# Optimization experiments

Measured on AMD Instinct MI355X. Metric: run time of the kernel, lower is better.

The kernel has to match this reference:

```python
import jax, jax.numpy as jnp
import numpy as np

IN_FEATURES = 256
OUT_FEATURES = 128
ALPHA = 0.2  # LeakyReLU negative slope
NEG_INF = -9e15
N_NODES = 8192


def _xavier_uniform(key, shape, gain):
    fan_in, fan_out = shape[0], shape[1]
    limit = gain * np.sqrt(6.0 / (fan_in + fan_out))
    return jax.random.uniform(key, shape, jnp.float32, -limit, limit)


def setup_inputs() -> dict:
    key = jax.random.key(0)
    k_h, k_adj, k_W, k_a = jax.random.split(key, 4)
    h = jax.random.normal(k_h, (N_NODES, IN_FEATURES), dtype=jnp.float32)
    adj = jax.random.randint(k_adj, (N_NODES, N_NODES), 0, 2, dtype=jnp.int32)
    W = _xavier_uniform(k_W, (IN_FEATURES, OUT_FEATURES), gain=1.414)
    a = _xavier_uniform(k_a, (2 * OUT_FEATURES, 1), gain=1.414)
    return {"h": h, "adj": adj, "W": W, "a": a}


def reference(h, adj, W, a):
    # Wh: (N, F_out)
    Wh = h @ W
    # Decompose a = [a1; a2]; e_ij = leakyrelu(Wh_i . a1 + Wh_j . a2)
    # == the original concat([Wh_i, Wh_j]) @ a, without the O(N^2*2F) tensor.
    a1 = a[:OUT_FEATURES, 0]  # (F_out,)
    a2 = a[OUT_FEATURES:, 0]  # (F_out,)
    src = Wh @ a1  # (N,)
    dst = Wh @ a2  # (N,)
    e = jax.nn.leaky_relu(src[:, None] + dst[None, :], negative_slope=ALPHA)  # (N, N)
    attention = jnp.where(adj > 0, e, NEG_INF)
    attention = jax.nn.softmax(attention, axis=1)
    # dropout p=0.0 (eval) -> identity
    h_prime = attention @ Wh  # (N, F_out)
    return jax.nn.elu(h_prime)  # concat=True
```

## Files before the change

kernel.cpp:

```cpp
#include <hip/hip_runtime.h>

#define N_NODES 8192
#define IN_F    256
#define OUT_F   128
#define ALPHA_S 0.2f

typedef __attribute__((ext_vector_type(8))) short  short8;
typedef __attribute__((ext_vector_type(4))) short  short4v;
typedef __attribute__((ext_vector_type(4))) float  floatx4;
typedef __attribute__((ext_vector_type(4))) int    intx4;
typedef __attribute__((ext_vector_type(4))) float  fx4;

static __device__ __forceinline__ short f2bf(float f) {
    union { float f; unsigned int i; } u; u.f = f;
    unsigned int r = u.i + 0x7FFFu + ((u.i >> 16) & 1u);
    return (short)(r >> 16);
}

__global__ __launch_bounds__(512) void k_wh(
    const float* __restrict__ h,
    const float* __restrict__ W,
    const float* __restrict__ a,
    short* __restrict__ WhT,
    float* __restrict__ src,
    float* __restrict__ dst)
{
    __shared__ short Wt[OUT_F][IN_F + 8];
    __shared__ short htile[32][IN_F + 8];
    __shared__ float q1s[IN_F], q2s[IN_F];
    __shared__ short wh_t[OUT_F][40];

    const int t      = threadIdx.x;
    const int lane   = t & 63;
    const int wave   = t >> 6;
    const int r_base = blockIdx.x * 32;

#pragma unroll
    for (int rep = 0; rep < 4; ++rep) {
        const int idx = rep * 8192 + t * 16;
        const int k   = idx >> 7;
        const int f   = idx & 127;
        fx4 w0 = *(const fx4*)(W + idx);
        fx4 w1 = *(const fx4*)(W + idx + 4);
        fx4 w2 = *(const fx4*)(W + idx + 8);
        fx4 w3 = *(const fx4*)(W + idx + 12);
        fx4 a10 = *(const fx4*)(a + f);
        fx4 a11 = *(const fx4*)(a + f + 4);
        fx4 a12 = *(const fx4*)(a + f + 8);
        fx4 a13 = *(const fx4*)(a + f + 12);
        fx4 a20 = *(const fx4*)(a + OUT_F + f);
        fx4 a21 = *(const fx4*)(a + OUT_F + f + 4);
        fx4 a22 = *(const fx4*)(a + OUT_F + f + 8);
        fx4 a23 = *(const fx4*)(a + OUT_F + f + 12);
        float p1 = 0.f, p2 = 0.f;
#pragma unroll
        for (int e = 0; e < 4; ++e) {
            p1 = fmaf(w0[e], a10[e], p1); p2 = fmaf(w0[e], a20[e], p2);
            p1 = fmaf(w1[e], a11[e], p1); p2 = fmaf(w1[e], a21[e], p2);
            p1 = fmaf(w2[e], a12[e], p1); p2 = fmaf(w2[e], a22[e], p2);
            p1 = fmaf(w3[e], a13[e], p1); p2 = fmaf(w3[e], a23[e], p2);
        }
#pragma unroll
        for (int e = 0; e < 4; ++e) {
            Wt[f + e][k]      = f2bf(w0[e]);
            Wt[f + 4 + e][k]  = f2bf(w1[e]);
            Wt[f + 8 + e][k]  = f2bf(w2[e]);
            Wt[f + 12 + e][k] = f2bf(w3[e]);
        }
#pragma unroll
        for (int m = 1; m < 8; m <<= 1) {
            p1 += __shfl_xor(p1, m, 64);
            p2 += __shfl_xor(p2, m, 64);
        }
        if ((t & 7) == 0) { q1s[k] = p1; q2s[k] = p2; }
    }

    const int r0   = t >> 4;
    const int fgrp = t & 15;
    const int k0   = fgrp * 16;
    fx4 h0, h1, h2, h3;
    {
        const float* hp = h + (size_t)(r_base + r0) * IN_F + k0;
        h0 = *(const fx4*)hp; h1 = *(const fx4*)(hp + 4);
        h2 = *(const fx4*)(hp + 8); h3 = *(const fx4*)(hp + 12);
        short8 b0, b1;
#pragma unroll
        for (int e = 0; e < 4; ++e) {
            b0[e]     = f2bf(h0[e]); b0[4 + e] = f2bf(h1[e]);
            b1[e]     = f2bf(h2[e]); b1[4 + e] = f2bf(h3[e]);
        }
        *(short8*)&htile[r0][k0]     = b0;
        *(short8*)&htile[r0][k0 + 8] = b1;
    }
    __syncthreads();

    {
        float sp = 0.f, dp = 0.f;
#pragma unroll
        for (int e = 0; e < 4; ++e) {
            sp = fmaf(h0[e], q1s[k0 + e], sp);      dp = fmaf(h0[e], q2s[k0 + e], dp);
            sp = fmaf(h1[e], q1s[k0 + 4 + e], sp);  dp = fmaf(h1[e], q2s[k0 + 4 + e], dp);
            sp = fmaf(h2[e], q1s[k0 + 8 + e], sp);  dp = fmaf(h2[e], q2s[k0 + 8 + e], dp);
            sp = fmaf(h3[e], q1s[k0 + 12 + e], sp); dp = fmaf(h3[e], q2s[k0 + 12 + e], dp);
        }
#pragma unroll
        for (int m = 1; m < 16; m <<= 1) {
            sp += __shfl_xor(sp, m, 64);
            dp += __shfl_xor(dp, m, 64);
        }
        if (fgrp == 0) { src[r_base + r0] = sp; dst[r_base + r0] = dp; }
    }

    const int ln15 = lane & 15;
    const int q    = lane >> 4;
    const int f0   = wave * 16;
    floatx4 c0 = {0.f, 0.f, 0.f, 0.f};
    floatx4 c1 = {0.f, 0.f, 0.f, 0.f};
#pragma unroll
    for (int s = 0; s < 8; ++s) {
        short8 bf  = *(const short8*)&Wt[f0 + ln15][s * 32 + q * 8];
        short8 a0f = *(const short8*)&htile[ln15][s * 32 + q * 8];
        short8 a1f = *(const short8*)&htile[16 + ln15][s * 32 + q * 8];
        c0 = __builtin_amdgcn_mfma_f32_16x16x32_bf16(a0f, bf, c0, 0, 0, 0);
        c1 = __builtin_amdgcn_mfma_f32_16x16x32_bf16(a1f, bf, c1, 0, 0, 0);
    }
    {
        short4v p0, p1;
#pragma unroll
        for (int r = 0; r < 4; ++r) { p0[r] = f2bf(c0[r]); p1[r] = f2bf(c1[r]); }
        *(short4v*)&wh_t[f0 + ln15][q * 4]      = p0;
        *(short4v*)&wh_t[f0 + ln15][16 + q * 4] = p1;
    }
    __syncthreads();
    {
        const int f    = t >> 2;
        const int half = t & 3;
        *(short8*)(WhT + (size_t)f * N_NODES + r_base + half * 8) =
            *(const short8*)&wh_t[f][half * 8];
    }
}

#define BM 32
#define BK 128
#define WPAD (BK + 8)
#define JCH 2048
#define NIT2 (JCH / BK)

__global__ __launch_bounds__(512, 4) void k_attn(
    const int*   __restrict__ adj,
    const short* __restrict__ WhT,
    const float* __restrict__ src,
    const float* __restrict__ dstv,
    float* __restrict__ numer_part,
    float* __restrict__ denom_part)
{
    __shared__ short wbuf[2][BM * WPAD];

    const int t    = threadIdx.x;
    const int lane = t & 63;
    const int wave = t >> 6;
    const int rg   = blockIdx.x >> 2;
    const int jc   = blockIdx.x & 3;
    const int r0   = rg * BM;
    const int jb   = jc * JCH;

    const int sm  = t >> 4;
    const int sk0 = (t & 15) * 8;
    const float srow = src[r0 + sm];
    const int*   abase = adj  + (size_t)(r0 + sm) * N_NODES + jb + sk0;
    const float* dbase = dstv + jb + sk0;

    const int ln15 = lane & 15;
    const int q    = lane >> 4;
    const int f0   = wave * 16;
    const short* bbase = WhT + (size_t)(f0 + ln15) * N_NODES + jb + q * 8;

    floatx4 acc0 = {0.f, 0.f, 0.f, 0.f};
    floatx4 acc1 = {0.f, 0.f, 0.f, 0.f};
    floatx4 dac0 = {0.f, 0.f, 0.f, 0.f};
    floatx4 dac1 = {0.f, 0.f, 0.f, 0.f};
    short8 ones;
#pragma unroll
    for (int j = 0; j < 8; ++j) ones[j] = (short)0x3F80;

    intx4 m0 = *(const intx4*)abase;
    intx4 m1 = *(const intx4*)(abase + 4);
    fx4   d0 = *(const fx4*)dbase;
    fx4   d1 = *(const fx4*)(dbase + 4);

    for (int it = 0; it < NIT2; ++it) {
        const int p = it & 1;
        short8 wv;
#pragma unroll
        for (int e = 0; e < 4; ++e) {
            float x = srow + d0[e];
            float l = fmaxf(x, ALPHA_S * x);
            wv[e] = (m0[e] > 0) ? f2bf(__expf(l)) : (short)0;
        }
#pragma unroll
        for (int e = 0; e < 4; ++e) {
            float x = srow + d1[e];
            float l = fmaxf(x, ALPHA_S * x);
            wv[4 + e] = (m1[e] > 0) ? f2bf(__expf(l)) : (short)0;
        }
        *(short8*)&wbuf[p][sm * WPAD + sk0] = wv;
        if (it + 1 < NIT2) {
            const int o = (it + 1) * BK;
            m0 = *(const intx4*)(abase + o);
            m1 = *(const intx4*)(abase + o + 4);
            d0 = *(const fx4*)(dbase + o);
            d1 = *(const fx4*)(dbase + o + 4);
        }
        __syncthreads();
        const short* ab = &wbuf[p][ln15 * WPAD + q * 8];
        const short* bb = bbase + it * BK;
#pragma unroll
        for (int ks = 0; ks < 4; ++ks) {
            short8 afr0 = *(const short8*)(ab + ks * 32);
            short8 afr1 = *(const short8*)(ab + 16 * WPAD + ks * 32);
            short8 bfr  = *(const short8*)(bb + ks * 32);
            acc0 = __builtin_amdgcn_mfma_f32_16x16x32_bf16(afr0, bfr, acc0, 0, 0, 0);
            acc1 = __builtin_amdgcn_mfma_f32_16x16x32_bf16(afr1, bfr, acc1, 0, 0, 0);
            if (wave == 0) {
                dac0 = __builtin_amdgcn_mfma_f32_16x16x32_bf16(afr0, ones, dac0, 0, 0, 0);
                dac1 = __builtin_amdgcn_mfma_f32_16x16x32_bf16(afr1, ones, dac1, 0, 0, 0);
            }
        }
    }

    float* np = numer_part + ((size_t)jc * N_NODES + r0) * OUT_F;
#pragma unroll
    for (int r = 0; r < 4; ++r) {
        np[(size_t)(q * 4 + r) * OUT_F + f0 + ln15]      = acc0[r];
        np[(size_t)(16 + q * 4 + r) * OUT_F + f0 + ln15] = acc1[r];
    }
    if (wave == 0 && ln15 == 0) {
        float* dp = denom_part + (size_t)jc * N_NODES + r0;
#pragma unroll
        for (int r = 0; r < 4; ++r) {
            dp[q * 4 + r]      = dac0[r];
            dp[16 + q * 4 + r] = dac1[r];
        }
    }
}

__global__ void k_final(const float* __restrict__ numer_part,
                        const float* __restrict__ denom_part,
                        float* __restrict__ out) {
    const int idx = blockIdx.x * 256 + threadIdx.x;
    const int row = idx >> 7;
    float v  = 0.f, dn = 0.f;
#pragma unroll
    for (int jc = 0; jc < 4; ++jc) {
        v  += numer_part[(size_t)jc * N_NODES * OUT_F + idx];
        dn += denom_part[(size_t)jc * N_NODES + row];
    }
    v = (dn != 0.f) ? (v / dn) : 0.f;
    v = v > 0.f ? v : (__expf(v) - 1.f);
    out[idx] = v;
}

extern "C" void kernel_launch(void* const* d_in, const int* in_sizes, int n_in,
                              void* d_out, int out_size, void* d_ws, size_t ws_size,
                              hipStream_t stream) {
    const float* h   = (const float*)d_in[0];
    const int*   adj = (const int*)d_in[1];
    const float* W   = (const float*)d_in[2];
    const float* a   = (const float*)d_in[3];
    float* out = (float*)d_out;

    char*  ws    = (char*)d_ws;
    float* denom_part = (float*)ws;
    short* WhT        = (short*)(ws + (128 << 10));
    float* src        = (float*)(ws + (128 << 10) + (2 << 20));
    float* dst        = src + N_NODES;
    float* numer_part = (float*)(ws + (4 << 20));

    k_wh   <<<256, 512, 0, stream>>>(h, W, a, WhT, src, dst);
    k_attn <<<1024, 512, 0, stream>>>(adj, WhT, src, dst, numer_part, denom_part);
    k_final<<<4096, 256, 0, stream>>>(numer_part, denom_part, out);
}
```

Before: 405.5 us.

## Drop split-K partials, fuse normalize+ELU into attention kernel with 1024-thread blocks

The attention kernel no longer splits the neighbor dimension into four chunks with separate partial buffers. Each block now owns 32 rows, loops over all 8192 columns, and uses 16 waves (two row groups by eight feature slices). Normalization and ELU are applied in the epilogue, which removes the final reduction kernel and the partial-buffer traffic. The grid shrinks from 1024 to 256 blocks, so each block runs a much longer serial loop. On a GPU with 256 CUs this gives roughly one large block per CU, which may reduce latency hiding.

```diff
diff --git a/kernel.cpp b/kernel.cpp
--- a/kernel.cpp
+++ b/kernel.cpp
@@ -143,121 +143,87 @@
 #define BM 32
 #define BK 128
 #define WPAD (BK + 8)
-#define JCH 2048
-#define NIT2 (JCH / BK)
-
-__global__ __launch_bounds__(512, 4) void k_attn(
+#define NIT (N_NODES / BK)
+
+__global__ __launch_bounds__(1024, 4) void k_attn(
     const int*   __restrict__ adj,
     const short* __restrict__ WhT,
     const float* __restrict__ src,
     const float* __restrict__ dstv,
-    float* __restrict__ numer_part,
-    float* __restrict__ denom_part)
+    float* __restrict__ out)
 {
     __shared__ short wbuf[2][BM * WPAD];
+    __shared__ float denom_s[BM];
 
     const int t    = threadIdx.x;
     const int lane = t & 63;
     const int wave = t >> 6;
-    const int rg   = blockIdx.x >> 2;
-    const int jc   = blockIdx.x & 3;
-    const int r0   = rg * BM;
-    const int jb   = jc * JCH;
-
-    const int sm  = t >> 4;
-    const int sk0 = (t & 15) * 8;
+    const int r0   = blockIdx.x * BM;
+
+    const int sm  = t >> 5;
+    const int sk0 = (t & 31) * 4;
     const float srow = src[r0 + sm];
-    const int*   abase = adj  + (size_t)(r0 + sm) * N_NODES + jb + sk0;
-    const float* dbase = dstv + jb + sk0;
+    const int*   abase = adj  + (size_t)(r0 + sm) * N_NODES + sk0;
+    const float* dbase = dstv + sk0;
 
     const int ln15 = lane & 15;
     const int q    = lane >> 4;
-    const int f0   = wave * 16;
-    const short* bbase = WhT + (size_t)(f0 + ln15) * N_NODES + jb + q * 8;
-
-    floatx4 acc0 = {0.f, 0.f, 0.f, 0.f};
-    floatx4 acc1 = {0.f, 0.f, 0.f, 0.f};
-    floatx4 dac0 = {0.f, 0.f, 0.f, 0.f};
-    floatx4 dac1 = {0.f, 0.f, 0.f, 0.f};
+    const int rg   = wave >> 3;
+    const int f0   = (wave & 7) * 16;
+    const short* bbase = WhT + (size_t)(f0 + ln15) * N_NODES + q * 8;
+
+    floatx4 acc = {0.f, 0.f, 0.f, 0.f};
+    floatx4 dac = {0.f, 0.f, 0.f, 0.f};
     short8 ones;
 #pragma unroll
     for (int j = 0; j < 8; ++j) ones[j] = (short)0x3F80;
 
     intx4 m0 = *(const intx4*)abase;
-    intx4 m1 = *(const intx4*)(abase + 4);
     fx4   d0 = *(const fx4*)dbase;
-    fx4   d1 = *(const fx4*)(dbase + 4);
-
-    for (int it = 0; it < NIT2; ++it) {
+
+    for (int it = 0; it < NIT; ++it) {
         const int p = it & 1;
-        short8 wv;
+        short4v wv;
 #pragma unroll
         for (int e = 0; e < 4; ++e) {
             float x = srow + d0[e];
             float l = fmaxf(x, ALPHA_S * x);
             wv[e] = (m0[e] > 0) ? f2bf(__expf(l)) : (short)0;
         }
-#pragma unroll
-        for (int e = 0; e < 4; ++e) {
-            float x = srow + d1[e];
-            float l = fmaxf(x, ALPHA_S * x);
-            wv[4 + e] = (m1[e] > 0) ? f2bf(__expf(l)) : (short)0;
-        }
-        *(short8*)&wbuf[p][sm * WPAD + sk0] = wv;
-        if (it + 1 < NIT2) {
+        *(short4v*)&wbuf[p][sm * WPAD + sk0] = wv;
+        if (it + 1 < NIT) {
             const int o = (it + 1) * BK;
             m0 = *(const intx4*)(abase + o);
-            m1 = *(const intx4*)(abase + o + 4);
             d0 = *(const fx4*)(dbase + o);
-            d1 = *(const fx4*)(dbase + o + 4);
         }
         __syncthreads();
-        const short* ab = &wbuf[p][ln15 * WPAD + q * 8];
+        const short* ab = &wbuf[p][(rg * 16 + ln15) * WPAD + q * 8];
         const short* bb = bbase + it * BK;
 #pragma unroll
         for (int ks = 0; ks < 4; ++ks) {
-            short8 afr0 = *(const short8*)(ab + ks * 32);
-            short8 afr1 = *(const short8*)(ab + 16 * WPAD + ks * 32);
-            short8 bfr  = *(const short8*)(bb + ks * 32);
-            acc0 = __builtin_amdgcn_mfma_f32_16x16x32_bf16(afr0, bfr, acc0, 0, 0, 0);
-            acc1 = __builtin_amdgcn_mfma_f32_16x16x32_bf16(afr1, bfr, acc1, 0, 0, 0);
-            if (wave == 0) {
-                dac0 = __builtin_amdgcn_mfma_f32_16x16x32_bf16(afr0, ones, dac0, 0, 0, 0);
-                dac1 = __builtin_amdgcn_mfma_f32_16x16x32_bf16(afr1, ones, dac1, 0, 0, 0);
-            }
-        }
-    }
-
-    float* np = numer_part + ((size_t)jc * N_NODES + r0) * OUT_F;
+            short8 afr = *(const short8*)(ab + ks * 32);
+            short8 bfr = *(const short8*)(bb + ks * 32);
+            acc = __builtin_amdgcn_mfma_f32_16x16x32_bf16(afr, bfr, acc, 0, 0, 0);
+            if ((wave & 7) == 0)
+                dac = __builtin_amdgcn_mfma_f32_16x16x32_bf16(afr, ones, dac, 0, 0, 0);
+        }
+    }
+
+    if ((wave & 7) == 0 && ln15 == 0) {
+#pragma unroll
+        for (int r = 0; r < 4; ++r) denom_s[rg * 16 + q * 4 + r] = dac[r];
+    }
+    __syncthreads();
+
+    float* op = out + (size_t)(r0 + rg * 16) * OUT_F + f0 + ln15;
 #pragma unroll
     for (int r = 0; r < 4; ++r) {
-        np[(size_t)(q * 4 + r) * OUT_F + f0 + ln15]      = acc0[r];
-        np[(size_t)(16 + q * 4 + r) * OUT_F + f0 + ln15] = acc1[r];
-    }
-    if (wave == 0 && ln15 == 0) {
-        float* dp = denom_part + (size_t)jc * N_NODES + r0;
-#pragma unroll
-        for (int r = 0; r < 4; ++r) {
-            dp[q * 4 + r]      = dac0[r];
-            dp[16 + q * 4 + r] = dac1[r];
-        }
-    }
-}
-
-__global__ void k_final(const float* __restrict__ numer_part,
-                        const float* __restrict__ denom_part,
-                        float* __restrict__ out) {
-    const int idx = blockIdx.x * 256 + threadIdx.x;
-    const int row = idx >> 7;
-    float v  = 0.f, dn = 0.f;
-#pragma unroll
-    for (int jc = 0; jc < 4; ++jc) {
-        v  += numer_part[(size_t)jc * N_NODES * OUT_F + idx];
-        dn += denom_part[(size_t)jc * N_NODES + row];
-    }
-    v = (dn != 0.f) ? (v / dn) : 0.f;
-    v = v > 0.f ? v : (__expf(v) - 1.f);
-    out[idx] = v;
+        float dn = denom_s[rg * 16 + q * 4 + r];
+        float v  = acc[r];
+        v = (dn != 0.f) ? (v / dn) : 0.f;
+        v = v > 0.f ? v : (__expf(v) - 1.f);
+        op[(size_t)(q * 4 + r) * OUT_F] = v;
+    }
 }
 
 extern "C" void kernel_launch(void* const* d_in, const int* in_sizes, int n_in,
@@ -269,14 +235,11 @@
     const float* a   = (const float*)d_in[3];
     float* out = (float*)d_out;
 
-    char*  ws    = (char*)d_ws;
-    float* denom_part = (float*)ws;
-    short* WhT        = (short*)(ws + (128 << 10));
-    float* src        = (float*)(ws + (128 << 10) + (2 << 20));
-    float* dst        = src + N_NODES;
-    float* numer_part = (float*)(ws + (4 << 20));
-
-    k_wh   <<<256, 512, 0, stream>>>(h, W, a, WhT, src, dst);
-    k_attn <<<1024, 512, 0, stream>>>(adj, WhT, src, dst, numer_part, denom_part);
-    k_final<<<4096, 256, 0, stream>>>(numer_part, denom_part, out);
-}
+    char*  ws  = (char*)d_ws;
+    short* WhT = (short*)ws;
+    float* src = (float*)(ws + (2 << 20));
+    float* dst = src + N_NODES;
+
+    k_wh  <<<256,  512, 0, stream>>>(h, W, a, WhT, src, dst);
+    k_attn<<<256, 1024, 0, stream>>>(adj, WhT, src, dst, out);
+}
```

Measured after the change: 455.2 us. 12.2% more time.
